# Performance work log

Measured on AMD Instinct MI355X. Metric: run time of the kernel, lower is better.

## Reference

```python
import jax, jax.numpy as jnp
import numpy as np

R = 512      # latent dim
M = 4        # center dimensionality
L = 256      # number of cluster centers
B = 8192     # batch
SIGMA_EPS = 1e-4


def setup_inputs() -> dict:
    key = jax.random.key(0)
    kx, kc = jax.random.split(key)
    x = jax.random.normal(kx, (B, R), dtype=jnp.float32)
    c = jax.random.normal(kc, (M, L), dtype=jnp.float32)   # codebook centers
    sigma = jnp.full((1,), 5.0, dtype=jnp.float32)         # trainable temperature
    return {"x": x, "c": c, "sigma": sigma}


def reference(x, c, sigma):
    b = x.shape[0]
    nf = R // M
    z = x.reshape(b, nf, M)                                # (b, nf, m)
    sig = jax.nn.relu(sigma[0]) + SIGMA_EPS
    # squared distances ||z - c||^2 over m, expanded to avoid (b,nf,m,L) materialization
    z_sq = jnp.sum(z * z, axis=-1, keepdims=True)          # (b, nf, 1)
    c_sq = jnp.sum(c * c, axis=0)                          # (L,)
    zc = jnp.einsum('bnm,ml->bnl', z, c)                   # (b, nf, L)
    dist = z_sq - 2.0 * zc + c_sq[None, None, :]           # (b, nf, L)
    q = jax.nn.softmax(-sig * dist, axis=-1)               # soft assignments (b, nf, L)
    out = jnp.einsum('bnl,ml->bnm', q, c)                  # weighted centers (b, nf, m)
    return out.reshape(b, R)
```

## Files before the change

kernel.cpp:

```cpp
#include <hip/hip_runtime.h>
#include <math.h>

#define RDIM 512
#define MDIM 4
#define LDIM 256
#define BDIM 8192
#define NROWS (BDIM * (RDIM / MDIM))
#define SIGMA_EPS 1e-4f
#define LOG2E 1.4426950408889634f

typedef _Float16 half4_t __attribute__((ext_vector_type(4)));
typedef _Float16 half8_t __attribute__((ext_vector_type(8)));
typedef __fp16   fp16x2_t __attribute__((ext_vector_type(2)));
typedef float    float4_t __attribute__((ext_vector_type(4)));

#define NRT (NROWS / 16)
#define MAIN_BLOCKS 2048
#define WPB 4
#define NT (NRT / (MAIN_BLOCKS * WPB))

__global__ void prep_kernel(const float* __restrict__ c, const float* __restrict__ sigma,
                            _Float16* __restrict__ a1w, _Float16* __restrict__ a2w) {
  const int gid  = blockIdx.x * 256 + threadIdx.x;
  const int lane = gid & 63;
  const int q4   = lane >> 4;
  const int m    = lane & 15;
  const float sig   = fmaxf(sigma[0], 0.0f) + SIGMA_EPS;
  const float sigL  = sig * LOG2E;
  const float sig2L = 2.0f * sigL;
  if (gid < 1024) {
    const int t = gid >> 6;
    const int l = t * 16 + m;
    float cv[4];
    cv[0] = c[l]; cv[1] = c[256 + l]; cv[2] = c[512 + l]; cv[3] = c[768 + l];
    _Float16 uh[4], ul[4];
    #pragma unroll
    for (int i = 0; i < 4; ++i) {
      float u = sig2L * cv[i];
      uh[i] = (_Float16)u;
      ul[i] = (_Float16)(u - (float)uh[i]);
    }
    float bias = -sigL * fmaf(cv[0], cv[0], fmaf(cv[1], cv[1], fmaf(cv[2], cv[2], cv[3] * cv[3])));
    _Float16 bh = (_Float16)bias;
    _Float16 bl = (_Float16)(bias - (float)bh);
    #pragma unroll
    for (int j = 0; j < 4; ++j) {
      _Float16 v;
      if      (q4 <  2) v = uh[j];
      else if (q4 == 2) v = ul[j];
      else              v = (j == 0) ? bh : ((j == 1) ? bl : (_Float16)1.0f);
      a1w[(t * 64 + lane) * 4 + j] = v;
    }
  } else if (gid < 1536) {
    const int p = (gid - 1024) >> 6;
    #pragma unroll
    for (int j = 0; j < 8; ++j) {
      int center = 32 * p + 16 * (j >> 2) + 4 * q4 + (j & 3);
      _Float16 v = (_Float16)0.0f;
      if (m < 4)       v = (_Float16)c[m * 256 + center];
      else if (m == 4) v = (_Float16)1.0f;
      a2w[(p * 64 + lane) * 8 + j] = v;
    }
  }
}

union U2H4 { uint2 u; half4_t h; };
union H4X2 { fp16x2_t e[4]; half8_t h8; };

__global__ __launch_bounds__(256, 4) void sq_mfma_kernel(
    const float4* __restrict__ x4,
    const _Float16* __restrict__ a1w,
    const _Float16* __restrict__ a2w,
    float4* __restrict__ out4) {
  const int tid  = threadIdx.x;
  const int lane = tid & 63;
  const int wave = tid >> 6;
  const int q4   = lane >> 4;
  const int zr   = lane & 15;

  half4_t a1[16];
  half8_t a2[8];
  const half4_t* a1p = (const half4_t*)a1w;
  const half8_t* a2p = (const half8_t*)a2w;
  #pragma unroll
  for (int t = 0; t < 16; ++t) a1[t] = a1p[t * 64 + lane];
  #pragma unroll
  for (int p = 0; p < 8; ++p) a2[p] = a2p[p * 64 + lane];

  const int gw = blockIdx.x * WPB + wave;
  const float4_t zero4 = {0.f, 0.f, 0.f, 0.f};
  const unsigned one_one = 0x3C003C00u;

  for (int it = 0; it < NT; ++it) {
    const int rowbase = (gw * NT + it) * 16;

    const float4 z = x4[rowbase + zr];
    fp16x2_t zh01 = __builtin_amdgcn_cvt_pkrtz(z.x, z.y);
    fp16x2_t zh23 = __builtin_amdgcn_cvt_pkrtz(z.z, z.w);
    fp16x2_t zl01 = __builtin_amdgcn_cvt_pkrtz(z.x - (float)zh01[0], z.y - (float)zh01[1]);
    fp16x2_t zl23 = __builtin_amdgcn_cvt_pkrtz(z.z - (float)zh23[0], z.w - (float)zh23[1]);
    const unsigned zh01u = __builtin_bit_cast(unsigned, zh01);
    const unsigned zh23u = __builtin_bit_cast(unsigned, zh23);
    const unsigned zl01u = __builtin_bit_cast(unsigned, zl01);
    const unsigned zl23u = __builtin_bit_cast(unsigned, zl23);

    const unsigned w0 = (q4 == 1) ? zl01u : ((q4 == 3) ? one_one : zh01u);
    const unsigned w1A = (q4 == 3) ? 0u : ((q4 == 1) ? zl23u : zh23u);
    U2H4 b1a; b1a.u = make_uint2(w0, w1A);

    float mx = -3.0e38f;
    #pragma unroll
    for (int t = 0; t < 16; ++t) {
      float4_t s = __builtin_amdgcn_mfma_f32_16x16x16f16(a1[t], b1a.h, zero4, 0, 0, 0);
      mx = fmaxf(fmaxf(mx, fmaxf(s[0], s[1])), fmaxf(s[2], s[3]));
    }
    mx = fmaxf(mx, __shfl_xor(mx, 16));
    mx = fmaxf(mx, __shfl_xor(mx, 32));

    float mhf = (float)(_Float16)mx;
    fp16x2_t nm = __builtin_amdgcn_cvt_pkrtz(-mhf, -(mx - mhf));
    const unsigned w1B = (q4 == 3) ? __builtin_bit_cast(unsigned, nm) : w1A;
    U2H4 b1b; b1b.u = make_uint2(w0, w1B);

    float4_t d2 = zero4;
    #pragma unroll
    for (int p = 0; p < 8; ++p) {
      float4_t sa = __builtin_amdgcn_mfma_f32_16x16x16f16(a1[2 * p],     b1b.h, zero4, 0, 0, 0);
      float4_t sb = __builtin_amdgcn_mfma_f32_16x16x16f16(a1[2 * p + 1], b1b.h, zero4, 0, 0, 0);
      H4X2 b2;
      b2.e[0] = __builtin_amdgcn_cvt_pkrtz(__builtin_amdgcn_exp2f(sa[0]), __builtin_amdgcn_exp2f(sa[1]));
      b2.e[1] = __builtin_amdgcn_cvt_pkrtz(__builtin_amdgcn_exp2f(sa[2]), __builtin_amdgcn_exp2f(sa[3]));
      b2.e[2] = __builtin_amdgcn_cvt_pkrtz(__builtin_amdgcn_exp2f(sb[0]), __builtin_amdgcn_exp2f(sb[1]));
      b2.e[3] = __builtin_amdgcn_cvt_pkrtz(__builtin_amdgcn_exp2f(sb[2]), __builtin_amdgcn_exp2f(sb[3]));
      d2 = __builtin_amdgcn_mfma_f32_16x16x32_f16(a2[p], b2.h8, d2, 0, 0, 0);
    }

    float den = __shfl(d2[0], zr + 16);
    if (lane < 16) {
      float r = __builtin_amdgcn_rcpf(den);
      float4 o = make_float4(d2[0] * r, d2[1] * r, d2[2] * r, d2[3] * r);
      out4[rowbase + zr] = o;
    }
  }
}

extern "C" void kernel_launch(void* const* d_in, const int* in_sizes, int n_in,
                              void* d_out, int out_size, void* d_ws, size_t ws_size,
                              hipStream_t stream) {
  const float4* x4    = (const float4*)d_in[0];
  const float*  c     = (const float*)d_in[1];
  const float*  sigma = (const float*)d_in[2];
  float4*       out4  = (float4*)d_out;

  _Float16* a1w = (_Float16*)d_ws;
  _Float16* a2w = a1w + 16 * 64 * 4;

  prep_kernel<<<6, 256, 0, stream>>>(c, sigma, a1w, a2w);
  sq_mfma_kernel<<<MAIN_BLOCKS, 256, 0, stream>>>(x4, a1w, a2w, out4);
}
```

Measured before the change: 114.7 us.

## Replace max pass with analytic softmax shift and bf16 second-stage MFMA

Removes the first 16-MFMA pass that computed the per-row maximum logit. Instead it shifts the logits by sigma*||z||^2 minus a fixed headroom, which bounds the exponent analytically because the logit sigma*(||z||^2 - dist) is at most sigma*||z||^2. To keep the wider exponent range safe, exponentials are truncated to bf16 with byte permutes rather than converted to fp16. The centers are split into hi/lo bf16 pairs, which doubles the second-stage MFMAs and the a2 registers. The trade is more register pressure and bf16 precision loss on the weights, and the fixed headroom could underflow when distances are large.

```diff
diff --git a/kernel.cpp b/kernel.cpp
--- a/kernel.cpp
+++ b/kernel.cpp
@@ -8,9 +8,10 @@
 #define NROWS (BDIM * (RDIM / MDIM))
 #define SIGMA_EPS 1e-4f
 #define LOG2E 1.4426950408889634f
+#define SHIFT_HEADROOM 96.0f
 
 typedef _Float16 half4_t __attribute__((ext_vector_type(4)));
-typedef _Float16 half8_t __attribute__((ext_vector_type(8)));
+typedef short    short8_t __attribute__((ext_vector_type(8)));
 typedef __fp16   fp16x2_t __attribute__((ext_vector_type(2)));
 typedef float    float4_t __attribute__((ext_vector_type(4)));
 
@@ -19,8 +20,13 @@
 #define WPB 4
 #define NT (NRT / (MAIN_BLOCKS * WPB))
 
+static __device__ __host__ inline unsigned short bf16_rne(float f) {
+  unsigned u = __builtin_bit_cast(unsigned, f);
+  return (unsigned short)((u + 0x7FFFu + ((u >> 16) & 1u)) >> 16);
+}
+
 __global__ void prep_kernel(const float* __restrict__ c, const float* __restrict__ sigma,
-                            _Float16* __restrict__ a1w, _Float16* __restrict__ a2w) {
+                            _Float16* __restrict__ a1w, unsigned short* __restrict__ a2w) {
   const int gid  = blockIdx.x * 256 + threadIdx.x;
   const int lane = gid & 63;
   const int q4   = lane >> 4;
@@ -51,26 +57,38 @@
       else              v = (j == 0) ? bh : ((j == 1) ? bl : (_Float16)1.0f);
       a1w[(t * 64 + lane) * 4 + j] = v;
     }
-  } else if (gid < 1536) {
+  } else if (gid < 2048) {
     const int p = (gid - 1024) >> 6;
+    const int pc = p & 7;
+    const bool hi = (p < 8);
     #pragma unroll
     for (int j = 0; j < 8; ++j) {
-      int center = 32 * p + 16 * (j >> 2) + 4 * q4 + (j & 3);
-      _Float16 v = (_Float16)0.0f;
-      if (m < 4)       v = (_Float16)c[m * 256 + center];
-      else if (m == 4) v = (_Float16)1.0f;
+      int center = 32 * pc + 16 * (j >> 2) + 4 * q4 + (j & 3);
+      unsigned short v = 0;
+      if (m < 4) {
+        float cf = c[m * 256 + center];
+        unsigned short h = bf16_rne(cf);
+        if (hi) v = h;
+        else {
+          float res = cf - __builtin_bit_cast(float, (unsigned)h << 16);
+          v = bf16_rne(res);
+        }
+      } else if (m == 4) {
+        v = hi ? (unsigned short)0x3F80 : (unsigned short)0;
+      }
       a2w[(p * 64 + lane) * 8 + j] = v;
     }
   }
 }
 
 union U2H4 { uint2 u; half4_t h; };
-union H4X2 { fp16x2_t e[4]; half8_t h8; };
+union U4S8 { uint4 u; short8_t s; };
 
 __global__ __launch_bounds__(256, 4) void sq_mfma_kernel(
     const float4* __restrict__ x4,
     const _Float16* __restrict__ a1w,
-    const _Float16* __restrict__ a2w,
+    const unsigned short* __restrict__ a2w,
+    const float* __restrict__ sigma,
     float4* __restrict__ out4) {
   const int tid  = threadIdx.x;
   const int lane = tid & 63;
@@ -78,14 +96,16 @@
   const int q4   = lane >> 4;
   const int zr   = lane & 15;
 
+  const float sigL = (fmaxf(sigma[0], 0.0f) + SIGMA_EPS) * LOG2E;
+
   half4_t a1[16];
-  half8_t a2[8];
+  short8_t a2[16];
   const half4_t* a1p = (const half4_t*)a1w;
-  const half8_t* a2p = (const half8_t*)a2w;
+  const short8_t* a2p = (const short8_t*)a2w;
   #pragma unroll
   for (int t = 0; t < 16; ++t) a1[t] = a1p[t * 64 + lane];
   #pragma unroll
-  for (int p = 0; p < 8; ++p) a2[p] = a2p[p * 64 + lane];
+  for (int p = 0; p < 16; ++p) a2[p] = a2p[p * 64 + lane];
 
   const int gw = blockIdx.x * WPB + wave;
   const float4_t zero4 = {0.f, 0.f, 0.f, 0.f};
@@ -104,35 +124,39 @@
     const unsigned zl01u = __builtin_bit_cast(unsigned, zl01);
     const unsigned zl23u = __builtin_bit_cast(unsigned, zl23);
 
+    float U = sigL * fmaf(z.x, z.x, fmaf(z.y, z.y, fmaf(z.z, z.z, z.w * z.w))) - SHIFT_HEADROOM;
+    float Uh = (float)(_Float16)U;
+    fp16x2_t nU = __builtin_amdgcn_cvt_pkrtz(-Uh, -(U - Uh));
+
     const unsigned w0 = (q4 == 1) ? zl01u : ((q4 == 3) ? one_one : zh01u);
-    const unsigned w1A = (q4 == 3) ? 0u : ((q4 == 1) ? zl23u : zh23u);
-    U2H4 b1a; b1a.u = make_uint2(w0, w1A);
-
-    float mx = -3.0e38f;
-    #pragma unroll
-    for (int t = 0; t < 16; ++t) {
-      float4_t s = __builtin_amdgcn_mfma_f32_16x16x16f16(a1[t], b1a.h, zero4, 0, 0, 0);
-      mx = fmaxf(fmaxf(mx, fmaxf(s[0], s[1])), fmaxf(s[2], s[3]));
-    }
-    mx = fmaxf(mx, __shfl_xor(mx, 16));
-    mx = fmaxf(mx, __shfl_xor(mx, 32));
-
-    float mhf = (float)(_Float16)mx;
-    fp16x2_t nm = __builtin_amdgcn_cvt_pkrtz(-mhf, -(mx - mhf));
-    const unsigned w1B = (q4 == 3) ? __builtin_bit_cast(unsigned, nm) : w1A;
-    U2H4 b1b; b1b.u = make_uint2(w0, w1B);
+    const unsigned w1 = (q4 == 3) ? __builtin_bit_cast(unsigned, nU)
+                                  : ((q4 == 1) ? zl23u : zh23u);
+    U2H4 b1; b1.u = make_uint2(w0, w1);
 
     float4_t d2 = zero4;
     #pragma unroll
     for (int p = 0; p < 8; ++p) {
-      float4_t sa = __builtin_amdgcn_mfma_f32_16x16x16f16(a1[2 * p],     b1b.h, zero4, 0, 0, 0);
-      float4_t sb = __builtin_amdgcn_mfma_f32_16x16x16f16(a1[2 * p + 1], b1b.h, zero4, 0, 0, 0);
-      H4X2 b2;
-      b2.e[0] = __builtin_amdgcn_cvt_pkrtz(__builtin_amdgcn_exp2f(sa[0]), __builtin_amdgcn_exp2f(sa[1]));
-      b2.e[1] = __builtin_amdgcn_cvt_pkrtz(__builtin_amdgcn_exp2f(sa[2]), __builtin_amdgcn_exp2f(sa[3]));
-      b2.e[2] = __builtin_amdgcn_cvt_pkrtz(__builtin_amdgcn_exp2f(sb[0]), __builtin_amdgcn_exp2f(sb[1]));
-      b2.e[3] = __builtin_amdgcn_cvt_pkrtz(__builtin_amdgcn_exp2f(sb[2]), __builtin_amdgcn_exp2f(sb[3]));
-      d2 = __builtin_amdgcn_mfma_f32_16x16x32_f16(a2[p], b2.h8, d2, 0, 0, 0);
+      float4_t sa = __builtin_amdgcn_mfma_f32_16x16x16f16(a1[2 * p],     b1.h, zero4, 0, 0, 0);
+      float4_t sb = __builtin_amdgcn_mfma_f32_16x16x16f16(a1[2 * p + 1], b1.h, zero4, 0, 0, 0);
+      float e0 = __builtin_amdgcn_exp2f(sa[0]);
+      float e1 = __builtin_amdgcn_exp2f(sa[1]);
+      float e2 = __builtin_amdgcn_exp2f(sa[2]);
+      float e3 = __builtin_amdgcn_exp2f(sa[3]);
+      float e4 = __builtin_amdgcn_exp2f(sb[0]);
+      float e5 = __builtin_amdgcn_exp2f(sb[1]);
+      float e6 = __builtin_amdgcn_exp2f(sb[2]);
+      float e7 = __builtin_amdgcn_exp2f(sb[3]);
+      U4S8 b2;
+      b2.u.x = __builtin_amdgcn_perm(__builtin_bit_cast(unsigned, e1),
+                                     __builtin_bit_cast(unsigned, e0), 0x07060302u);
+      b2.u.y = __builtin_amdgcn_perm(__builtin_bit_cast(unsigned, e3),
+                                     __builtin_bit_cast(unsigned, e2), 0x07060302u);
+      b2.u.z = __builtin_amdgcn_perm(__builtin_bit_cast(unsigned, e5),
+                                     __builtin_bit_cast(unsigned, e4), 0x07060302u);
+      b2.u.w = __builtin_amdgcn_perm(__builtin_bit_cast(unsigned, e7),
+                                     __builtin_bit_cast(unsigned, e6), 0x07060302u);
+      d2 = __builtin_amdgcn_mfma_f32_16x16x32_bf16(a2[p],     b2.s, d2, 0, 0, 0);
+      d2 = __builtin_amdgcn_mfma_f32_16x16x32_bf16(a2[p + 8], b2.s, d2, 0, 0, 0);
     }
 
     float den = __shfl(d2[0], zr + 16);
@@ -152,9 +176,9 @@
   const float*  sigma = (const float*)d_in[2];
   float4*       out4  = (float4*)d_out;
 
-  _Float16* a1w = (_Float16*)d_ws;
-  _Float16* a2w = a1w + 16 * 64 * 4;
+  _Float16*       a1w = (_Float16*)d_ws;
+  unsigned short* a2w = (unsigned short*)(a1w + 16 * 64 * 4);
 
-  prep_kernel<<<6, 256, 0, stream>>>(c, sigma, a1w, a2w);
-  sq_mfma_kernel<<<MAIN_BLOCKS, 256, 0, stream>>>(x4, a1w, a2w, out4);
+  prep_kernel<<<8, 256, 0, stream>>>(c, sigma, a1w, a2w);
+  sq_mfma_kernel<<<MAIN_BLOCKS, 256, 0, stream>>>(x4, a1w, a2w, sigma, out4);
 }
```

After: 103.3 us. -10.0%, faster.
